# Kernel tuning notes

Hardware: AMD Instinct MI355X
Metric: run time of the kernel (lower is better)

The kernel has to match this reference:

```python
import jax, jax.numpy as jnp
import numpy as np

EPS = 1e-16
S = 20  # amino-acid alphabet size, hardcoded in original (reshape to (-1,20,20))


def make_rate_matrix(R, p):
    """R: (n,S,S) symmetric, zero diag; p: (n,S) equilibrium. Returns normalized Q: (n,S,S)."""
    Q = R * p[:, None, :]
    diag = jnp.sum(Q, axis=-1, keepdims=True)          # (n,S,1)
    Q = Q - diag * jnp.eye(S, dtype=p.dtype)           # put -rowsum on diagonal
    mue = jnp.sum(p[..., None] * diag, axis=-2, keepdims=True)  # (n,1,1) expected mutation rate
    return Q / jnp.maximum(mue, EPS)


def setup_inputs() -> dict:
    key = jax.random.key(0)
    k1, k2, k3, k4, k5 = jax.random.split(key, 5)
    m, b, L, k, num_rates = 2, 512, 512, 2, 512
    sequences = jax.random.randint(k1, (m, b, L), 0, S, dtype=jnp.int32)
    rate_indices = jax.random.randint(k2, (m, b), 0, num_rates, dtype=jnp.int32)
    tau_kernel = jax.random.normal(k3, (m, num_rates), dtype=jnp.float32) - 3.0  # rate_init = const(-3)
    exchangeability_kernel = jax.random.normal(k4, (m, k, S, S), dtype=jnp.float32)
    equilibrium_kernel = jax.random.normal(k5, (m, k, S), dtype=jnp.float32)
    return {"sequences": sequences, "rate_indices": rate_indices, "tau_kernel": tau_kernel,
            "exchangeability_kernel": exchangeability_kernel, "equilibrium_kernel": equilibrium_kernel}


def reference(sequences, rate_indices, tau_kernel, exchangeability_kernel, equilibrium_kernel):
    m, k = exchangeability_kernel.shape[:2]
    b = sequences.shape[1]
    # make_R: symmetrize, softplus, zero diagonal
    R = jax.nn.softplus(0.5 * (exchangeability_kernel + jnp.swapaxes(exchangeability_kernel, -1, -2)))
    R = R * (1.0 - jnp.eye(S, dtype=R.dtype))
    # make_p: softmax equilibrium
    p = jax.nn.softmax(equilibrium_kernel, axis=-1)
    # normalized rate matrices Q: (m,k,S,S)
    Q = make_rate_matrix(R.reshape(-1, S, S), p.reshape(-1, S)).reshape(m, k, S, S)
    # make_tau: gather per-sequence time, softplus
    tau = jax.nn.softplus(tau_kernel[jnp.arange(m)[:, None], rate_indices])  # (m,b)
    # tau*Q and batched matrix exponential: (m,b,k,S,S)
    tauQ = tau[:, :, None, None, None] * Q[:, None]
    P = jax.scipy.linalg.expm(tauQ)
    # embedding-lookup combine: ancprobs[m,b,l,k,:] = P[m,b,k,seq[m,b,l],:]
    P_t = jnp.transpose(P, (0, 1, 3, 2, 4))  # (m,b,S,k,S)
    mi = jnp.arange(m)[:, None, None]
    bi = jnp.arange(b)[None, :, None]
    ancprobs = P_t[mi, bi, sequences]  # (m,b,L,k,S)
    return ancprobs
```

## Files before the change

kernel.cpp:

```cpp
#include <hip/hip_runtime.h>
#include <math.h>

#define SA 20
#define KDIM 2
#define MDIM 2
#define BDIM 512
#define LDIM 512
#define NRATES 512
#define MATW (SA * SA)
#define NCH (LDIM * KDIM * SA / 4)
#define SPLIT 4
#define GCH (NCH / SPLIT)
#define LSLICE (LDIM / SPLIT)

__device__ __forceinline__ float softplusf(float x) {
    return fmaxf(x, 0.0f) + log1pf(expf(-fabsf(x)));
}

__device__ __forceinline__ void mmB(float* C, const float* A, const float* Bl) {
    #pragma unroll
    for (int j = 0; j < SA; ++j) C[j] = 0.0f;
    #pragma unroll
    for (int t = 0; t < SA; ++t) {
        const float a = A[t];
        const float4* row = reinterpret_cast<const float4*>(Bl + t * SA);
        #pragma unroll
        for (int q = 0; q < 5; ++q) {
            float4 b = row[q];
            C[4*q+0] = fmaf(a, b.x, C[4*q+0]);
            C[4*q+1] = fmaf(a, b.y, C[4*q+1]);
            C[4*q+2] = fmaf(a, b.z, C[4*q+2]);
            C[4*q+3] = fmaf(a, b.w, C[4*q+3]);
        }
    }
}

__device__ __forceinline__ void stageRow(float* dst, const float* T, int row, bool act) {
    if (act) {
        float4* d4 = reinterpret_cast<float4*>(dst + row * SA);
        #pragma unroll
        for (int q = 0; q < 5; ++q)
            d4[q] = make_float4(T[4*q+0], T[4*q+1], T[4*q+2], T[4*q+3]);
    }
}

__global__ __launch_bounds__(64) void expm_kernel(
    const int*   __restrict__ rateIdx,
    const float* __restrict__ tauk,
    const float* __restrict__ Ek,
    const float* __restrict__ eqk,
    float*       __restrict__ Pg)
{
    __shared__ float sStage[KDIM * MATW];

    const int lane = threadIdx.x;
    const int mb   = blockIdx.x;
    const int mm   = mb >> 9;

    const int  half = lane >> 5;
    const int  row  = lane & 31;
    const bool act  = row < SA;
    const int  mk   = mm * KDIM + half;
    const int  r0   = act ? row : 0;
    float* stage = sStage + half * MATW;

    float e = act ? eqk[mk * SA + row] : -INFINITY;
    float mx = e;
    #pragma unroll
    for (int off = 16; off; off >>= 1) mx = fmaxf(mx, __shfl_xor(mx, off, 32));
    float ex = act ? expf(e - mx) : 0.0f;
    float sm = ex;
    #pragma unroll
    for (int off = 16; off; off >>= 1) sm += __shfl_xor(sm, off, 32);
    float p_i = ex / sm;

    float A[SA];
    float dg = 0.0f;
    #pragma unroll
    for (int j = 0; j < SA; ++j) {
        float pj = __shfl(p_i, j, 32);
        float e1 = Ek[(mk * SA + r0) * SA + j];
        float e2 = Ek[(mk * SA + j) * SA + r0];
        float r  = (j == row) ? 0.0f : softplusf(0.5f * (e1 + e2));
        float q  = r * pj;
        A[j] = q;
        dg  += q;
    }
    float t_ = act ? p_i * dg : 0.0f;
    #pragma unroll
    for (int off = 16; off; off >>= 1) t_ += __shfl_xor(t_, off, 32);
    const float inv = 1.0f / fmaxf(t_, 1e-16f);

    const float tau = softplusf(tauk[mm * NRATES + rateIdx[mb]]);
    const float sc  = tau * inv;
    #pragma unroll
    for (int j = 0; j < SA; ++j)
        A[j] = act ? ((j == row) ? -dg * sc : A[j] * sc) : 0.0f;

    float rn = 0.0f;
    #pragma unroll
    for (int j = 0; j < SA; ++j) rn += fabsf(A[j]);
    #pragma unroll
    for (int off = 16; off; off >>= 1) rn = fmaxf(rn, __shfl_xor(rn, off, 32));
    int s = 0;
    if (rn > 1.0f) s = (int)ceilf(log2f(rn));
    if (s < 0) s = 0;
    if (s > 30) s = 30;
    const float scale = exp2f((float)(-s));
    #pragma unroll
    for (int j = 0; j < SA; ++j) A[j] *= scale;
    const int smax = max(s, __shfl_xor(s, 32, 64));

    float A2[SA], A3[SA], T[SA];
    stageRow(stage, A, row, act);
    mmB(A2, A, stage);
    mmB(A3, A2, stage);
    #pragma unroll
    for (int j = 0; j < SA; ++j) {
        float id = (j == row) ? 1.0f : 0.0f;
        T[j] = (1.0f/6.0f)*id + (1.0f/24.0f)*A[j] + (1.0f/120.0f)*A2[j] + (1.0f/720.0f)*A3[j];
    }
    stageRow(stage, T, row, act);
    {
        float P1[SA];
        mmB(P1, A3, stage);
        #pragma unroll
        for (int j = 0; j < SA; ++j) {
            float id = (j == row) ? 1.0f : 0.0f;
            T[j] = P1[j] + id + A[j] + 0.5f * A2[j];
        }
    }
    for (int it = 0; it < smax; ++it) {
        stageRow(stage, T, row, act);
        float Tn[SA];
        mmB(Tn, T, stage);
        const bool doit = it < s;
        #pragma unroll
        for (int j = 0; j < SA; ++j) T[j] = doit ? Tn[j] : T[j];
    }

    if (act) {
        float4* d4 = reinterpret_cast<float4*>(Pg + ((size_t)mb * KDIM + half) * MATW + row * SA);
        #pragma unroll
        for (int q = 0; q < 5; ++q)
            d4[q] = make_float4(T[4*q+0], T[4*q+1], T[4*q+2], T[4*q+3]);
    }
}

__global__ __launch_bounds__(256, 8) void gather_kernel(
    const int*   __restrict__ seqg,
    const float* __restrict__ Pg,
    float*       __restrict__ out)
{
    __shared__ float4 sP4[KDIM * SA * 5];
    __shared__ int    sSeq[LSLICE];

    const int tid = threadIdx.x;
    const int mb  = blockIdx.x >> 2;
    const int qq  = blockIdx.x & 3;

    if (tid < 200) {
        sP4[tid] = reinterpret_cast<const float4*>(Pg + (size_t)mb * KDIM * MATW)[tid];
    } else if (tid >= 224) {
        reinterpret_cast<int4*>(sSeq)[tid - 224] =
            reinterpret_cast<const int4*>(seqg + (size_t)mb * LDIM + qq * LSLICE)[tid - 224];
    }
    __syncthreads();

    float4* o4 = reinterpret_cast<float4*>(out) + (size_t)mb * NCH + qq * GCH;
    #pragma unroll
    for (int i = 0; i < 5; ++i) {
        const int c  = tid + i * 256;
        const int l  = c / 10;
        const int ch = c - l * 10;
        const int kk = (ch >= 5) ? 1 : 0;
        const int c4 = ch - kk * 5;
        o4[c] = sP4[kk * 100 + sSeq[l] * 5 + c4];
    }
}

extern "C" void kernel_launch(void* const* d_in, const int* in_sizes, int n_in,
                              void* d_out, int out_size, void* d_ws, size_t ws_size,
                              hipStream_t stream) {
    const int*   seq  = (const int*)d_in[0];
    const int*   ridx = (const int*)d_in[1];
    const float* tauk = (const float*)d_in[2];
    const float* Ek   = (const float*)d_in[3];
    const float* eqk  = (const float*)d_in[4];
    float* out = (float*)d_out;
    float* Pg  = (float*)d_ws;

    expm_kernel<<<MDIM * BDIM, 64, 0, stream>>>(ridx, tauk, Ek, eqk, Pg);
    gather_kernel<<<MDIM * BDIM * SPLIT, 256, 0, stream>>>(seq, Pg, out);
}
```

Baseline: 118.7 us.

## Fuse expm and gather into one kernel with Horner Taylor expm

Merges the expm kernel and the gather kernel into a single launch. Each block recomputes the (m,k) rate matrices and the scaled expm in shared memory, then writes its half of the sequence rows. This removes the intermediate P round trip through global memory and one kernel launch. The series becomes a degree-6 Horner Taylor evaluation spread across 256 threads, and the scaling exponent now comes from a cheaper norm bound (2·max row sum). In exchange, every block duplicates the expm work (two blocks per sequence), and the output-writing phase is halved in parallelism compared with the previous split of 4.

```diff
diff --git a/kernel.cpp b/kernel.cpp
--- a/kernel.cpp
+++ b/kernel.cpp
@@ -8,174 +8,185 @@
 #define LDIM 512
 #define NRATES 512
 #define MATW (SA * SA)
+#define NEL (KDIM * MATW)
+#define SPLIT 2
 #define NCH (LDIM * KDIM * SA / 4)
-#define SPLIT 4
 #define GCH (NCH / SPLIT)
 #define LSLICE (LDIM / SPLIT)
+#define GITER (GCH / 256)
 
 __device__ __forceinline__ float softplusf(float x) {
     return fmaxf(x, 0.0f) + log1pf(expf(-fabsf(x)));
 }
 
-__device__ __forceinline__ void mmB(float* C, const float* A, const float* Bl) {
-    #pragma unroll
-    for (int j = 0; j < SA; ++j) C[j] = 0.0f;
-    #pragma unroll
-    for (int t = 0; t < SA; ++t) {
-        const float a = A[t];
-        const float4* row = reinterpret_cast<const float4*>(Bl + t * SA);
-        #pragma unroll
-        for (int q = 0; q < 5; ++q) {
-            float4 b = row[q];
-            C[4*q+0] = fmaf(a, b.x, C[4*q+0]);
-            C[4*q+1] = fmaf(a, b.y, C[4*q+1]);
-            C[4*q+2] = fmaf(a, b.z, C[4*q+2]);
-            C[4*q+3] = fmaf(a, b.w, C[4*q+3]);
-        }
-    }
-}
-
-__device__ __forceinline__ void stageRow(float* dst, const float* T, int row, bool act) {
-    if (act) {
-        float4* d4 = reinterpret_cast<float4*>(dst + row * SA);
-        #pragma unroll
-        for (int q = 0; q < 5; ++q)
-            d4[q] = make_float4(T[4*q+0], T[4*q+1], T[4*q+2], T[4*q+3]);
-    }
-}
-
-__global__ __launch_bounds__(64) void expm_kernel(
+__global__ __launch_bounds__(256) void ancprobs_lean_kernel(
+    const int*   __restrict__ seqg,
     const int*   __restrict__ rateIdx,
     const float* __restrict__ tauk,
     const float* __restrict__ Ek,
     const float* __restrict__ eqk,
-    float*       __restrict__ Pg)
-{
-    __shared__ float sStage[KDIM * MATW];
-
-    const int lane = threadIdx.x;
-    const int mb   = blockIdx.x;
-    const int mm   = mb >> 9;
-
-    const int  half = lane >> 5;
-    const int  row  = lane & 31;
-    const bool act  = row < SA;
-    const int  mk   = mm * KDIM + half;
-    const int  r0   = act ? row : 0;
-    float* stage = sStage + half * MATW;
-
-    float e = act ? eqk[mk * SA + row] : -INFINITY;
-    float mx = e;
-    #pragma unroll
-    for (int off = 16; off; off >>= 1) mx = fmaxf(mx, __shfl_xor(mx, off, 32));
-    float ex = act ? expf(e - mx) : 0.0f;
-    float sm = ex;
-    #pragma unroll
-    for (int off = 16; off; off >>= 1) sm += __shfl_xor(sm, off, 32);
-    float p_i = ex / sm;
-
-    float A[SA];
-    float dg = 0.0f;
-    #pragma unroll
-    for (int j = 0; j < SA; ++j) {
-        float pj = __shfl(p_i, j, 32);
-        float e1 = Ek[(mk * SA + r0) * SA + j];
-        float e2 = Ek[(mk * SA + j) * SA + r0];
-        float r  = (j == row) ? 0.0f : softplusf(0.5f * (e1 + e2));
-        float q  = r * pj;
-        A[j] = q;
-        dg  += q;
-    }
-    float t_ = act ? p_i * dg : 0.0f;
-    #pragma unroll
-    for (int off = 16; off; off >>= 1) t_ += __shfl_xor(t_, off, 32);
-    const float inv = 1.0f / fmaxf(t_, 1e-16f);
-
-    const float tau = softplusf(tauk[mm * NRATES + rateIdx[mb]]);
-    const float sc  = tau * inv;
-    #pragma unroll
-    for (int j = 0; j < SA; ++j)
-        A[j] = act ? ((j == row) ? -dg * sc : A[j] * sc) : 0.0f;
-
-    float rn = 0.0f;
-    #pragma unroll
-    for (int j = 0; j < SA; ++j) rn += fabsf(A[j]);
-    #pragma unroll
-    for (int off = 16; off; off >>= 1) rn = fmaxf(rn, __shfl_xor(rn, off, 32));
-    int s = 0;
-    if (rn > 1.0f) s = (int)ceilf(log2f(rn));
-    if (s < 0) s = 0;
-    if (s > 30) s = 30;
-    const float scale = exp2f((float)(-s));
-    #pragma unroll
-    for (int j = 0; j < SA; ++j) A[j] *= scale;
-    const int smax = max(s, __shfl_xor(s, 32, 64));
-
-    float A2[SA], A3[SA], T[SA];
-    stageRow(stage, A, row, act);
-    mmB(A2, A, stage);
-    mmB(A3, A2, stage);
-    #pragma unroll
-    for (int j = 0; j < SA; ++j) {
-        float id = (j == row) ? 1.0f : 0.0f;
-        T[j] = (1.0f/6.0f)*id + (1.0f/24.0f)*A[j] + (1.0f/120.0f)*A2[j] + (1.0f/720.0f)*A3[j];
-    }
-    stageRow(stage, T, row, act);
-    {
-        float P1[SA];
-        mmB(P1, A3, stage);
-        #pragma unroll
-        for (int j = 0; j < SA; ++j) {
-            float id = (j == row) ? 1.0f : 0.0f;
-            T[j] = P1[j] + id + A[j] + 0.5f * A2[j];
-        }
-    }
-    for (int it = 0; it < smax; ++it) {
-        stageRow(stage, T, row, act);
-        float Tn[SA];
-        mmB(Tn, T, stage);
-        const bool doit = it < s;
-        #pragma unroll
-        for (int j = 0; j < SA; ++j) T[j] = doit ? Tn[j] : T[j];
-    }
-
-    if (act) {
-        float4* d4 = reinterpret_cast<float4*>(Pg + ((size_t)mb * KDIM + half) * MATW + row * SA);
-        #pragma unroll
-        for (int q = 0; q < 5; ++q)
-            d4[q] = make_float4(T[4*q+0], T[4*q+1], T[4*q+2], T[4*q+3]);
-    }
-}
-
-__global__ __launch_bounds__(256, 8) void gather_kernel(
-    const int*   __restrict__ seqg,
-    const float* __restrict__ Pg,
     float*       __restrict__ out)
 {
-    __shared__ float4 sP4[KDIM * SA * 5];
-    __shared__ int    sSeq[LSLICE];
+    __shared__ __align__(16) float sA[NEL];
+    __shared__ __align__(16) float sB1[NEL];
+    __shared__ __align__(16) float sB2[NEL];
+    __shared__ int   sSeq[LSLICE];
+    __shared__ float sp[KDIM * SA];
+    __shared__ float sd[KDIM * SA];
+    __shared__ float sFac[KDIM];
+    __shared__ int   sS[KDIM];
+    __shared__ float sTau;
 
     const int tid = threadIdx.x;
-    const int mb  = blockIdx.x >> 2;
-    const int qq  = blockIdx.x & 3;
-
-    if (tid < 200) {
-        sP4[tid] = reinterpret_cast<const float4*>(Pg + (size_t)mb * KDIM * MATW)[tid];
-    } else if (tid >= 224) {
-        reinterpret_cast<int4*>(sSeq)[tid - 224] =
-            reinterpret_cast<const int4*>(seqg + (size_t)mb * LDIM + qq * LSLICE)[tid - 224];
-    }
-    __syncthreads();
-
-    float4* o4 = reinterpret_cast<float4*>(out) + (size_t)mb * NCH + qq * GCH;
+    const int mb  = blockIdx.x >> 1;
+    const int qq  = blockIdx.x & 1;
+    const int mm  = mb >> 9;
+
+    if (tid < 64)
+        reinterpret_cast<int4*>(sSeq)[tid] =
+            reinterpret_cast<const int4*>(seqg + (size_t)mb * LDIM + qq * LSLICE)[tid];
+    if (tid < 200)
+        reinterpret_cast<float4*>(sB1)[tid] =
+            reinterpret_cast<const float4*>(Ek + (size_t)mm * NEL)[tid];
+    if (tid >= 200 && tid < 240)
+        sp[tid - 200] = eqk[mm * KDIM * SA + (tid - 200)];
+    if (tid == 255)
+        sTau = softplusf(tauk[mm * NRATES + rateIdx[mb]]);
+    __syncthreads();
+
+    if (tid < 64) {
+        const int  half = tid >> 5;
+        const int  row  = tid & 31;
+        const bool act  = row < SA;
+        float e = act ? sp[half * SA + row] : -INFINITY;
+        float mx = e;
+        #pragma unroll
+        for (int off = 16; off; off >>= 1) mx = fmaxf(mx, __shfl_xor(mx, off, 32));
+        float ex = act ? expf(e - mx) : 0.0f;
+        float sm = ex;
+        #pragma unroll
+        for (int off = 16; off; off >>= 1) sm += __shfl_xor(sm, off, 32);
+        if (act) sd[half * SA + row] = ex / sm;
+    }
+    __syncthreads();
+
+    for (int e = tid; e < NEL; e += 256) {
+        const int kk  = (e >= MATW) ? 1 : 0;
+        const int idx = e - kk * MATW;
+        const int r   = idx / SA;
+        const int c   = idx - r * SA;
+        float v = 0.0f;
+        if (r != c) {
+            float e1 = sB1[kk * MATW + r * SA + c];
+            float e2 = sB1[kk * MATW + c * SA + r];
+            v = softplusf(0.5f * (e1 + e2)) * sd[kk * SA + c];
+        }
+        sA[e] = v;
+    }
+    __syncthreads();
+    if (tid < 40) sp[tid] = sd[tid];
+    __syncthreads();
+
+    if (tid < 64) {
+        const int  half = tid >> 5;
+        const int  row  = tid & 31;
+        const bool act  = row < SA;
+        float dg = 0.0f;
+        if (act) {
+            const float* rp = sA + half * MATW + row * SA;
+            #pragma unroll
+            for (int c = 0; c < SA; ++c) dg += rp[c];
+        }
+        float p_i = act ? sp[half * SA + row] : 0.0f;
+        float t_ = p_i * dg;
+        #pragma unroll
+        for (int off = 16; off; off >>= 1) t_ += __shfl_xor(t_, off, 32);
+        const float inv = 1.0f / fmaxf(t_, 1e-16f);
+        float rm = act ? dg : 0.0f;
+        #pragma unroll
+        for (int off = 16; off; off >>= 1) rm = fmaxf(rm, __shfl_xor(rm, off, 32));
+        const float tau = sTau;
+        const float n   = tau * inv * 2.0f * rm;
+        int s = 0;
+        if (n > 1.0f) s = (int)ceilf(log2f(n));
+        s = min(max(s, 0), 30);
+        if (act) sd[half * SA + row] = dg;
+        if (row == 0) {
+            sFac[half] = tau * inv * exp2f(-(float)s);
+            sS[half]   = s;
+        }
+    }
+    __syncthreads();
+
+    for (int e = tid; e < NEL; e += 256) {
+        const int kk  = (e >= MATW) ? 1 : 0;
+        const int idx = e - kk * MATW;
+        const int r   = idx / SA;
+        const int c   = idx - r * SA;
+        float a = ((r == c) ? -sd[kk * SA + r] : sA[e]) * sFac[kk];
+        sA[e]  = a;
+        sB1[e] = ((r == c) ? 1.0f : 0.0f) + a * (1.0f / 6.0f);
+    }
+    __syncthreads();
+
+    float* cur = sB1;
+    float* nxt = sB2;
     #pragma unroll
-    for (int i = 0; i < 5; ++i) {
+    for (int d = 5; d >= 1; --d) {
+        const float rd = 1.0f / (float)d;
+        for (int e = tid; e < NEL; e += 256) {
+            const int kk  = (e >= MATW) ? 1 : 0;
+            const int idx = e - kk * MATW;
+            const int r   = idx / SA;
+            const int c   = idx - r * SA;
+            const float* ar = sA  + kk * MATW + r * SA;
+            const float* uc = cur + kk * MATW + c;
+            float acc = 0.0f;
+            #pragma unroll
+            for (int t = 0; t < SA; ++t)
+                acc = fmaf(ar[t], uc[t * SA], acc);
+            nxt[e] = ((r == c) ? 1.0f : 0.0f) + acc * rd;
+        }
+        __syncthreads();
+        float* tmp = cur; cur = nxt; nxt = tmp;
+    }
+
+    const int s0 = sS[0], s1 = sS[1];
+    const int smax = max(s0, s1);
+    for (int it = 0; it < smax; ++it) {
+        for (int e = tid; e < NEL; e += 256) {
+            const int kk  = (e >= MATW) ? 1 : 0;
+            const int idx = e - kk * MATW;
+            const int r   = idx / SA;
+            const int c   = idx - r * SA;
+            const int sk  = kk ? s1 : s0;
+            float acc;
+            if (it < sk) {
+                const float* tr = cur + kk * MATW + r * SA;
+                const float* tc = cur + kk * MATW + c;
+                acc = 0.0f;
+                #pragma unroll
+                for (int t = 0; t < SA; ++t)
+                    acc = fmaf(tr[t], tc[t * SA], acc);
+            } else {
+                acc = cur[e];
+            }
+            nxt[e] = acc;
+        }
+        __syncthreads();
+        float* tmp = cur; cur = nxt; nxt = tmp;
+    }
+
+    const float4* pv = reinterpret_cast<const float4*>(cur);
+    float4* o4 = reinterpret_cast<float4*>(out) + (size_t)mb * NCH + (size_t)qq * GCH;
+    #pragma unroll
+    for (int i = 0; i < GITER; ++i) {
         const int c  = tid + i * 256;
         const int l  = c / 10;
         const int ch = c - l * 10;
         const int kk = (ch >= 5) ? 1 : 0;
         const int c4 = ch - kk * 5;
-        o4[c] = sP4[kk * 100 + sSeq[l] * 5 + c4];
+        o4[c] = pv[kk * 100 + sSeq[l] * 5 + c4];
     }
 }
 
@@ -188,8 +199,7 @@
     const float* Ek   = (const float*)d_in[3];
     const float* eqk  = (const float*)d_in[4];
     float* out = (float*)d_out;
-    float* Pg  = (float*)d_ws;
-
-    expm_kernel<<<MDIM * BDIM, 64, 0, stream>>>(ridx, tauk, Ek, eqk, Pg);
-    gather_kernel<<<MDIM * BDIM * SPLIT, 256, 0, stream>>>(seq, Pg, out);
+
+    ancprobs_lean_kernel<<<MDIM * BDIM * SPLIT, 256, 0, stream>>>(
+        seq, ridx, tauk, Ek, eqk, out);
 }
```

New measurement: 114.1 us. 3.8% less time.
